# Optimization experiments

Hardware: AMD Instinct MI355X
Metric: run time of the kernel (lower is better)

## Reference

```python
import jax, jax.numpy as jnp
import numpy as np

N = 100_000      # nodes
E = 1_600_000    # edges (avg degree 16)
IN, H, OUT = 128, 64, 32
G = 128          # graphs in batch
EPS = 1e-5


def setup_inputs() -> dict:
    key = jax.random.key(0)
    ks = jax.random.split(key, 12)
    x = jax.random.normal(ks[0], (N, IN), jnp.float32)
    edge_index = jax.random.randint(ks[1], (2, E), 0, N, dtype=jnp.int32)
    batch = jnp.sort(jax.random.randint(ks[2], (N,), 0, G, dtype=jnp.int32))
    # GCNConv weights (glorot-ish scaling), shared BatchNorm params, final linear
    W1 = jax.random.normal(ks[3], (IN, H), jnp.float32) / np.sqrt(IN)
    b1 = jnp.zeros((H,), jnp.float32)
    W2 = jax.random.normal(ks[4], (H, H), jnp.float32) / np.sqrt(H)
    b2 = jnp.zeros((H,), jnp.float32)
    gamma = jnp.ones((H,), jnp.float32)
    beta = jnp.zeros((H,), jnp.float32)
    linW = jax.random.normal(ks[5], (H, OUT), jnp.float32) / np.sqrt(H)
    linb = jnp.zeros((OUT,), jnp.float32)
    return dict(x=x, edge_index=edge_index, batch=batch, W1=W1, b1=b1,
                W2=W2, b2=b2, gamma=gamma, beta=beta, linW=linW, linb=linb)


def _gcn_edges(edge_index):
    # add self loops (PyG GCNConv default) and symmetric normalization
    loop = jnp.arange(N, dtype=edge_index.dtype)
    src = jnp.concatenate([edge_index[0], loop])
    dst = jnp.concatenate([edge_index[1], loop])
    deg = jax.ops.segment_sum(jnp.ones_like(src, jnp.float32), dst, num_segments=N)
    dis = jnp.where(deg > 0, jax.lax.rsqrt(deg), 0.0)
    norm = dis[src] * dis[dst]          # [E+N]
    return src, dst, norm


def _gcn_conv(h, W, b, src, dst, norm):
    h = h @ W                            # [N, out] small GEMM first (PyG order)
    msg = h[src] * norm[:, None]         # gather + edgewise normalize
    return jax.ops.segment_sum(msg, dst, num_segments=N) + b  # scatter-add


def _batchnorm(h, gamma, beta):
    # training-mode batch stats over nodes (biased variance, as torch BN)
    mean = h.mean(axis=0)
    var = jnp.mean((h - mean) ** 2, axis=0)
    return (h - mean) * jax.lax.rsqrt(var + EPS) * gamma + beta


def reference(x, edge_index, batch, W1, b1, W2, b2, gamma, beta, linW, linb):
    src, dst, norm = _gcn_edges(edge_index)
    h = jax.nn.relu(_batchnorm(_gcn_conv(x, W1, b1, src, dst, norm), gamma, beta))
    h = jax.nn.relu(_batchnorm(_gcn_conv(h, W2, b2, src, dst, norm), gamma, beta))
    # global mean pool over graph ids
    sums = jax.ops.segment_sum(h, batch, num_segments=G)
    cnts = jax.ops.segment_sum(jnp.ones((N,), h.dtype), batch, num_segments=G)
    pooled = sums / jnp.maximum(cnts, 1.0)[:, None]   # [G, H]
    return pooled @ linW + linb                        # [G, OUT]
```

## Files before the change

kernel.cpp:

```cpp
#include <hip/hip_runtime.h>

#define NNODES 100000
#define NEDGES 1600000
#define FIN 128
#define FH 64
#define FOUT 32
#define NGRAPH 128
#define EPSV 1e-5f

#define SCAN_BT 256
#define NBLK ((NNODES + SCAN_BT - 1) / SCAN_BT)

typedef unsigned short ushort_t;
typedef __attribute__((ext_vector_type(8))) short bf16x8;
typedef __attribute__((ext_vector_type(4))) float f32x4;

__device__ inline unsigned f2bf(float f) {
  union { float f; unsigned u; } x;
  x.f = f;
  return (x.u + 0x7fffu + ((x.u >> 16) & 1u)) >> 16;
}
__device__ inline float bflo(unsigned u) {
  union { unsigned u; float f; } x;
  x.u = u << 16;
  return x.f;
}
__device__ inline float bfhi(unsigned u) {
  union { unsigned u; float f; } x;
  x.u = u & 0xffff0000u;
  return x.f;
}


__global__ void k_deg_accum(const int* __restrict__ dst, int* __restrict__ deg) {
  const int SLICE = NNODES / 8;
  int xcd = blockIdx.x & 7;
  int lo = xcd * SLICE, hi = lo + SLICE;
  int chunk = blockIdx.x >> 3;
  int nchunk = gridDim.x >> 3;
  for (int i = chunk * blockDim.x + threadIdx.x; i < NEDGES; i += nchunk * blockDim.x) {
    int d = dst[i];
    if (d >= lo && d < hi) atomicAdd(&deg[d], 1);
  }
}


__global__ void k_blocksum(const int* __restrict__ deg, int* __restrict__ bsum) {
  __shared__ int ls[SCAN_BT];
  int b = blockIdx.x, t = threadIdx.x;
  int i = b * SCAN_BT + t;
  ls[t] = (i < NNODES) ? deg[i] : 0;
  __syncthreads();
  for (int s = SCAN_BT / 2; s > 0; s >>= 1) {
    if (t < s) ls[t] += ls[t + s];
    __syncthreads();
  }
  if (t == 0) bsum[b] = ls[0];
}

__global__ void k_scan_bsums(const int* __restrict__ bsum, int* __restrict__ boff) {
  __shared__ int ls[512];
  int t = threadIdx.x;
  int v = (t < NBLK) ? bsum[t] : 0;
  ls[t] = v;
  __syncthreads();
  for (int s = 1; s < 512; s <<= 1) {
    int add = (t >= s) ? ls[t - s] : 0;
    __syncthreads();
    ls[t] += add;
    __syncthreads();
  }
  if (t < NBLK) boff[t] = ls[t] - v;
}


__global__ void k_scan_final(const int* __restrict__ deg, const int* __restrict__ boff,
                             int* __restrict__ off, float* __restrict__ dis) {
  __shared__ int ls[SCAN_BT];
  int b = blockIdx.x, t = threadIdx.x;
  int i = b * SCAN_BT + t;
  int v = (i < NNODES) ? deg[i] : 0;
  ls[t] = v;
  __syncthreads();
  for (int s = 1; s < SCAN_BT; s <<= 1) {
    int add = (t >= s) ? ls[t - s] : 0;
    __syncthreads();
    ls[t] += add;
    __syncthreads();
  }
  if (i < NNODES) {
    off[i] = boff[b] + ls[t] - v;
    dis[i] = rsqrtf((float)v + 1.0f);
  }
  if (i == NNODES - 1) off[NNODES] = boff[b] + ls[t];
}


__global__ void k_fill(const int* __restrict__ src, const int* __restrict__ dst,
                       const int* __restrict__ off, int* __restrict__ cursor,
                       int* __restrict__ csr) {
  const int SLICE = NNODES / 8;
  int xcd = blockIdx.x & 7;
  int lo = xcd * SLICE, hi = lo + SLICE;
  int chunk = blockIdx.x >> 3;
  int nchunk = gridDim.x >> 3;
  for (int i = chunk * blockDim.x + threadIdx.x; i < NEDGES; i += nchunk * blockDim.x) {
    int d = dst[i];
    if (d >= lo && d < hi) {
      int p = atomicAdd(&cursor[d], 1);
      csr[off[d] + p] = src[i];
    }
  }
}


template <int K, bool BN>
__global__ void k_gemm_mfma(const float* __restrict__ A, const float* __restrict__ W,
                            const float* __restrict__ stats, const float* __restrict__ gamma,
                            const float* __restrict__ beta, const float* __restrict__ dis,
                            ushort_t* __restrict__ out) {
  const int WT = K + 8;
  __shared__ ushort_t wt[64 * (K + 8)];
  __shared__ float bn_sc[K], bn_sh[K];
  if (BN && threadIdx.x < K) {
    int f = threadIdx.x;
    float mean = stats[f] * (1.0f / NNODES);
    float var = stats[K + f] * (1.0f / NNODES) - mean * mean;
    float s = gamma[f] * rsqrtf(var + EPSV);
    bn_sc[f] = s;
    bn_sh[f] = beta[f] - mean * s;
  }
  for (int idx = threadIdx.x; idx < K * 64; idx += 256) {
    int k = idx >> 6, col = idx & 63;
    wt[col * WT + k] = (ushort_t)f2bf(W[idx]);
  }
  __syncthreads();

  int wave = threadIdx.x >> 6;
  int lane = threadIdx.x & 63;
  int rrow = lane & 15;
  int g = lane >> 4;
  int row0 = (blockIdx.x * 4 + wave) * 16;
  int arow = min(row0 + rrow, NNODES - 1);
  const float* a = A + (long long)arow * K;

  f32x4 acc0 = {0.f, 0.f, 0.f, 0.f}, acc1 = acc0, acc2 = acc0, acc3 = acc0;

#pragma unroll
  for (int ks = 0; ks < K / 32; ++ks) {
    int koff = ks * 32 + g * 8;
    float4 xa = *(const float4*)(a + koff);
    float4 xb = *(const float4*)(a + koff + 4);
    float xs[8] = {xa.x, xa.y, xa.z, xa.w, xb.x, xb.y, xb.z, xb.w};
    if (BN) {
#pragma unroll
      for (int j = 0; j < 8; ++j)
        xs[j] = fmaxf(fmaf(xs[j], bn_sc[koff + j], bn_sh[koff + j]), 0.0f);
    }
    bf16x8 af;
#pragma unroll
    for (int j = 0; j < 8; ++j) af[j] = (short)f2bf(xs[j]);
    bf16x8 b0 = *(const bf16x8*)&wt[(0 * 16 + rrow) * WT + koff];
    bf16x8 b1 = *(const bf16x8*)&wt[(1 * 16 + rrow) * WT + koff];
    bf16x8 b2 = *(const bf16x8*)&wt[(2 * 16 + rrow) * WT + koff];
    bf16x8 b3 = *(const bf16x8*)&wt[(3 * 16 + rrow) * WT + koff];
    acc0 = __builtin_amdgcn_mfma_f32_16x16x32_bf16(af, b0, acc0, 0, 0, 0);
    acc1 = __builtin_amdgcn_mfma_f32_16x16x32_bf16(af, b1, acc1, 0, 0, 0);
    acc2 = __builtin_amdgcn_mfma_f32_16x16x32_bf16(af, b2, acc2, 0, 0, 0);
    acc3 = __builtin_amdgcn_mfma_f32_16x16x32_bf16(af, b3, acc3, 0, 0, 0);
  }

  int orow0 = row0 + g * 4;
#pragma unroll
  for (int r = 0; r < 4; ++r) {
    int orow = orow0 + r;
    if (orow < NNODES) {
      float d = dis[orow];
      ushort_t* o = out + (long long)orow * FH + rrow;
      o[0] = (ushort_t)f2bf(acc0[r] * d);
      o[16] = (ushort_t)f2bf(acc1[r] * d);
      o[32] = (ushort_t)f2bf(acc2[r] * d);
      o[48] = (ushort_t)f2bf(acc3[r] * d);
    }
  }
}


__global__ void k_gather(const ushort_t* __restrict__ hs, const int* __restrict__ csr,
                         const int* __restrict__ off, const float* __restrict__ dis,
                         float* __restrict__ out, float* __restrict__ stats) {
  __shared__ float ls[2 * FH];
  int tid = threadIdx.x;
  if (tid < 2 * FH) ls[tid] = 0.0f;
  __syncthreads();
  int lane = tid & 63;
  int g = lane >> 4;
  int i = lane & 15;
  int wid = (blockIdx.x * blockDim.x + tid) >> 6;
  int nw = (gridDim.x * blockDim.x) >> 6;
  const int HALF = NNODES / 2;
  float s1x = 0, s1y = 0, s1z = 0, s1w = 0;
  float s2x = 0, s2y = 0, s2z = 0, s2w = 0;
  for (int p = wid; p < HALF; p += nw) {
    int dA = p, dB = p + HALF;
    int bA = off[dA], eA = off[dA + 1];
    int bB = off[dB], eB = off[dB + 1];
    uint2 suA = *(const uint2*)(hs + (long long)dA * FH + i * 4);
    uint2 suB = *(const uint2*)(hs + (long long)dB * FH + i * 4);
    float axA = (g == 0) ? bflo(suA.x) : 0.0f;
    float ayA = (g == 0) ? bfhi(suA.x) : 0.0f;
    float azA = (g == 0) ? bflo(suA.y) : 0.0f;
    float awA = (g == 0) ? bfhi(suA.y) : 0.0f;
    float axB = (g == 0) ? bflo(suB.x) : 0.0f;
    float ayB = (g == 0) ? bfhi(suB.x) : 0.0f;
    float azB = (g == 0) ? bflo(suB.y) : 0.0f;
    float awB = (g == 0) ? bfhi(suB.y) : 0.0f;
    int nA = (eA - bA + 15) >> 4, nB = (eB - bB + 15) >> 4;
    int niter = max(nA, nB);
    int lastA = max(eA - 1, 0), lastB = max(eB - 1, 0);
    int kA = bA + g, kB = bB + g;
    for (int j = 0; j < niter; ++j) {
      int a0 = kA + 16 * j, a1 = a0 + 4, a2 = a0 + 8, a3 = a0 + 12;
      int b0 = kB + 16 * j, b1 = b0 + 4, b2 = b0 + 8, b3 = b0 + 12;
      int cA0 = csr[min(a0, lastA)];
      int cA1 = csr[min(a1, lastA)];
      int cA2 = csr[min(a2, lastA)];
      int cA3 = csr[min(a3, lastA)];
      int cB0 = csr[min(b0, lastB)];
      int cB1 = csr[min(b1, lastB)];
      int cB2 = csr[min(b2, lastB)];
      int cB3 = csr[min(b3, lastB)];
      uint2 uA0 = *(const uint2*)(hs + (long long)cA0 * FH + i * 4);
      uint2 uA1 = *(const uint2*)(hs + (long long)cA1 * FH + i * 4);
      uint2 uA2 = *(const uint2*)(hs + (long long)cA2 * FH + i * 4);
      uint2 uA3 = *(const uint2*)(hs + (long long)cA3 * FH + i * 4);
      uint2 uB0 = *(const uint2*)(hs + (long long)cB0 * FH + i * 4);
      uint2 uB1 = *(const uint2*)(hs + (long long)cB1 * FH + i * 4);
      uint2 uB2 = *(const uint2*)(hs + (long long)cB2 * FH + i * 4);
      uint2 uB3 = *(const uint2*)(hs + (long long)cB3 * FH + i * 4);
      bool A0 = a0 < eA, A1 = a1 < eA, A2 = a2 < eA, A3 = a3 < eA;
      bool B0 = b0 < eB, B1 = b1 < eB, B2 = b2 < eB, B3 = b3 < eB;
      axA += (A0 ? bflo(uA0.x) : 0.0f) + (A1 ? bflo(uA1.x) : 0.0f) +
             (A2 ? bflo(uA2.x) : 0.0f) + (A3 ? bflo(uA3.x) : 0.0f);
      ayA += (A0 ? bfhi(uA0.x) : 0.0f) + (A1 ? bfhi(uA1.x) : 0.0f) +
             (A2 ? bfhi(uA2.x) : 0.0f) + (A3 ? bfhi(uA3.x) : 0.0f);
      azA += (A0 ? bflo(uA0.y) : 0.0f) + (A1 ? bflo(uA1.y) : 0.0f) +
             (A2 ? bflo(uA2.y) : 0.0f) + (A3 ? bflo(uA3.y) : 0.0f);
      awA += (A0 ? bfhi(uA0.y) : 0.0f) + (A1 ? bfhi(uA1.y) : 0.0f) +
             (A2 ? bfhi(uA2.y) : 0.0f) + (A3 ? bfhi(uA3.y) : 0.0f);
      axB += (B0 ? bflo(uB0.x) : 0.0f) + (B1 ? bflo(uB1.x) : 0.0f) +
             (B2 ? bflo(uB2.x) : 0.0f) + (B3 ? bflo(uB3.x) : 0.0f);
      ayB += (B0 ? bfhi(uB0.x) : 0.0f) + (B1 ? bfhi(uB1.x) : 0.0f) +
             (B2 ? bfhi(uB2.x) : 0.0f) + (B3 ? bfhi(uB3.x) : 0.0f);
      azB += (B0 ? bflo(uB0.y) : 0.0f) + (B1 ? bflo(uB1.y) : 0.0f) +
             (B2 ? bflo(uB2.y) : 0.0f) + (B3 ? bflo(uB3.y) : 0.0f);
      awB += (B0 ? bfhi(uB0.y) : 0.0f) + (B1 ? bfhi(uB1.y) : 0.0f) +
             (B2 ? bfhi(uB2.y) : 0.0f) + (B3 ? bfhi(uB3.y) : 0.0f);
    }
    axA += __shfl_xor(axA, 16); axA += __shfl_xor(axA, 32);
    ayA += __shfl_xor(ayA, 16); ayA += __shfl_xor(ayA, 32);
    azA += __shfl_xor(azA, 16); azA += __shfl_xor(azA, 32);
    awA += __shfl_xor(awA, 16); awA += __shfl_xor(awA, 32);
    axB += __shfl_xor(axB, 16); axB += __shfl_xor(axB, 32);
    ayB += __shfl_xor(ayB, 16); ayB += __shfl_xor(ayB, 32);
    azB += __shfl_xor(azB, 16); azB += __shfl_xor(azB, 32);
    awB += __shfl_xor(awB, 16); awB += __shfl_xor(awB, 32);
    float ddA = dis[dA], ddB = dis[dB];
    float oxA = axA * ddA, oyA = ayA * ddA, ozA = azA * ddA, owA = awA * ddA;
    float oxB = axB * ddB, oyB = ayB * ddB, ozB = azB * ddB, owB = awB * ddB;
    if (g < 2) {
      int d = (g == 0) ? dA : dB;
      float4 o4;
      o4.x = (g == 0) ? oxA : oxB;
      o4.y = (g == 0) ? oyA : oyB;
      o4.z = (g == 0) ? ozA : ozB;
      o4.w = (g == 0) ? owA : owB;
      *(float4*)(out + (long long)d * FH + i * 4) = o4;
    }
    s1x += oxA + oxB; s2x += oxA * oxA + oxB * oxB;
    s1y += oyA + oyB; s2y += oyA * oyA + oyB * oyB;
    s1z += ozA + ozB; s2z += ozA * ozA + ozB * ozB;
    s1w += owA + owB; s2w += owA * owA + owB * owB;
  }
  if (g == 0) {
    atomicAdd(&ls[i * 4 + 0], s1x);
    atomicAdd(&ls[i * 4 + 1], s1y);
    atomicAdd(&ls[i * 4 + 2], s1z);
    atomicAdd(&ls[i * 4 + 3], s1w);
    atomicAdd(&ls[FH + i * 4 + 0], s2x);
    atomicAdd(&ls[FH + i * 4 + 1], s2y);
    atomicAdd(&ls[FH + i * 4 + 2], s2z);
    atomicAdd(&ls[FH + i * 4 + 3], s2w);
  }
  __syncthreads();
  if (tid < 2 * FH) atomicAdd(&stats[tid], ls[tid]);
}


#define POOL_WAVES 1024

__global__ void k_pool(const float* __restrict__ h, const int* __restrict__ batch,
                       const float* __restrict__ stats, const float* __restrict__ gamma,
                       const float* __restrict__ beta, float* __restrict__ pooled,
                       float* __restrict__ cnt) {
  const int CHUNK = (NNODES + POOL_WAVES - 1) / POOL_WAVES;
  int lane = threadIdx.x & 63;
  int wid = (blockIdx.x * blockDim.x + threadIdx.x) >> 6;
  int start = wid * CHUNK;
  if (start >= NNODES) return;
  int end = min(start + CHUNK, NNODES);
  float mean = stats[lane] * (1.0f / NNODES);
  float var = stats[FH + lane] * (1.0f / NNODES) - mean * mean;
  float sc = gamma[lane] * rsqrtf(var + EPSV);
  float sh = beta[lane] - mean * sc;
  int cur = batch[start];
  float acc = 0.0f;
  int cl = 0;
  for (int n = start; n < end; ++n) {
    int g = batch[n];
    if (g != cur) {
      atomicAdd(&pooled[cur * FH + lane], acc);
      if (lane == 0) atomicAdd(&cnt[cur], (float)cl);
      acc = 0.0f;
      cl = 0;
      cur = g;
    }
    float v = fmaf(h[(long long)n * FH + lane], sc, sh);
    acc += fmaxf(v, 0.0f);
    ++cl;
  }
  atomicAdd(&pooled[cur * FH + lane], acc);
  if (lane == 0) atomicAdd(&cnt[cur], (float)cl);
}


__global__ void k_final(const float* __restrict__ pooled, const float* __restrict__ cnt,
                        const float* __restrict__ linW, const float* __restrict__ linb,
                        float* __restrict__ out) {
  int t = blockIdx.x * blockDim.x + threadIdx.x;
  if (t >= NGRAPH * FOUT) return;
  int g = t / FOUT, o = t % FOUT;
  float inv = 1.0f / fmaxf(cnt[g], 1.0f);
  float acc = linb[o];
#pragma unroll
  for (int k = 0; k < FH; ++k) acc = fmaf(pooled[g * FH + k] * inv, linW[k * FOUT + o], acc);
  out[t] = acc;
}

extern "C" void kernel_launch(void* const* d_in, const int* in_sizes, int n_in,
                              void* d_out, int out_size, void* d_ws, size_t ws_size,
                              hipStream_t stream) {
  const float* x = (const float*)d_in[0];
  const int* edge_index = (const int*)d_in[1];
  const int* batch = (const int*)d_in[2];
  const float* W1 = (const float*)d_in[3];
  const float* W2 = (const float*)d_in[5];
  const float* gamma = (const float*)d_in[7];
  const float* beta = (const float*)d_in[8];
  const float* linW = (const float*)d_in[9];
  const float* linb = (const float*)d_in[10];
  float* out = (float*)d_out;

  const int* esrc = edge_index;
  const int* edst = edge_index + NEDGES;

  ushort_t* bufA = (ushort_t*)d_ws;
  float* bufB = (float*)d_ws + (long long)NNODES * FH;
  float* dis = bufB + (long long)NNODES * FH;
  int* off = (int*)(dis + NNODES);
  int* csr = off + (NNODES + 1);
  int* bsum = csr + NEDGES;
  int* boff = bsum + NBLK;
  int* deg = boff + NBLK;
  int* cursor = deg + NNODES;
  float* stats1 = (float*)(cursor + NNODES);
  float* stats2 = stats1 + 2 * FH;
  float* pooled = stats2 + 2 * FH;
  float* cnt = pooled + NGRAPH * FH;

  const int BT = 256;
  const int gN = (NNODES + BT - 1) / BT;
  const int gM = (NNODES + 63) / 64;

  hipMemsetAsync(deg, 0,
                 (size_t)(2 * NNODES + 2 * 2 * FH + NGRAPH * FH + NGRAPH) * sizeof(int), stream);

  k_deg_accum<<<2048, BT, 0, stream>>>(edst, deg);
  k_blocksum<<<NBLK, SCAN_BT, 0, stream>>>(deg, bsum);
  k_scan_bsums<<<1, 512, 0, stream>>>(bsum, boff);
  k_scan_final<<<NBLK, SCAN_BT, 0, stream>>>(deg, boff, off, dis);
  k_fill<<<2048, BT, 0, stream>>>(esrc, edst, off, cursor, csr);

  k_gemm_mfma<FIN, false><<<gM, BT, 0, stream>>>(x, W1, nullptr, nullptr, nullptr, dis, bufA);
  k_gather<<<2048, BT, 0, stream>>>(bufA, csr, off, dis, bufB, stats1);

  k_gemm_mfma<FH, true><<<gM, BT, 0, stream>>>(bufB, W2, stats1, gamma, beta, dis, bufA);
  k_gather<<<2048, BT, 0, stream>>>(bufA, csr, off, dis, bufB, stats2);

  k_pool<<<POOL_WAVES * 64 / BT, BT, 0, stream>>>(bufB, batch, stats2, gamma, beta, pooled, cnt);
  k_final<<<(NGRAPH * FOUT + BT - 1) / BT, BT, 0, stream>>>(pooled, cnt, linW, linb, out);
}
```

Before: 418.3 us.

## Fuse CSR fill with first GEMM and widen gather to 8-feature lanes

Merges the CSR fill kernel and the first MFMA GEMM into one launch, with disjoint block ranges, so the two independent stages can overlap. Restructures the gather kernel so each lane handles 8 bf16 features with 16-byte loads over 8 edge groups, halving the load count per edge and changing the shuffle reduction. The fused launch shifts the block-to-XCD mapping of the fill section, and the gather init contains redundant code.

Measured after the change: 419.9 us. Within noise of the previous version (+0.4%).

```diff
diff --git a/kernel.cpp b/kernel.cpp
--- a/kernel.cpp
+++ b/kernel.cpp
@@ -10,6 +10,8 @@
 
 #define SCAN_BT 256
 #define NBLK ((NNODES + SCAN_BT - 1) / SCAN_BT)
+#define GM ((NNODES + 63) / 64)
+#define FILLBLK 2048
 
 typedef unsigned short ushort_t;
 typedef __attribute__((ext_vector_type(8))) short bf16x8;
@@ -73,7 +75,6 @@
   if (t < NBLK) boff[t] = ls[t] - v;
 }
 
-
 __global__ void k_scan_final(const int* __restrict__ deg, const int* __restrict__ boff,
                              int* __restrict__ off, float* __restrict__ dis) {
   __shared__ int ls[SCAN_BT];
@@ -96,29 +97,14 @@
 }
 
 
-__global__ void k_fill(const int* __restrict__ src, const int* __restrict__ dst,
-                       const int* __restrict__ off, int* __restrict__ cursor,
-                       int* __restrict__ csr) {
-  const int SLICE = NNODES / 8;
-  int xcd = blockIdx.x & 7;
-  int lo = xcd * SLICE, hi = lo + SLICE;
-  int chunk = blockIdx.x >> 3;
-  int nchunk = gridDim.x >> 3;
-  for (int i = chunk * blockDim.x + threadIdx.x; i < NEDGES; i += nchunk * blockDim.x) {
-    int d = dst[i];
-    if (d >= lo && d < hi) {
-      int p = atomicAdd(&cursor[d], 1);
-      csr[off[d] + p] = src[i];
-    }
-  }
-}
-
-
 template <int K, bool BN>
-__global__ void k_gemm_mfma(const float* __restrict__ A, const float* __restrict__ W,
-                            const float* __restrict__ stats, const float* __restrict__ gamma,
-                            const float* __restrict__ beta, const float* __restrict__ dis,
-                            ushort_t* __restrict__ out) {
+__device__ __forceinline__ void gemm_body(int bid, const float* __restrict__ A,
+                                          const float* __restrict__ W,
+                                          const float* __restrict__ stats,
+                                          const float* __restrict__ gamma,
+                                          const float* __restrict__ beta,
+                                          const float* __restrict__ dis,
+                                          ushort_t* __restrict__ out) {
   const int WT = K + 8;
   __shared__ ushort_t wt[64 * (K + 8)];
   __shared__ float bn_sc[K], bn_sh[K];
@@ -140,7 +126,7 @@
   int lane = threadIdx.x & 63;
   int rrow = lane & 15;
   int g = lane >> 4;
-  int row0 = (blockIdx.x * 4 + wave) * 16;
+  int row0 = (bid * 4 + wave) * 16;
   int arow = min(row0 + rrow, NNODES - 1);
   const float* a = A + (long long)arow * K;
 
@@ -185,6 +171,49 @@
   }
 }
 
+template <int K, bool BN>
+__global__ void k_gemm_mfma(const float* __restrict__ A, const float* __restrict__ W,
+                            const float* __restrict__ stats, const float* __restrict__ gamma,
+                            const float* __restrict__ beta, const float* __restrict__ dis,
+                            ushort_t* __restrict__ out) {
+  gemm_body<K, BN>(blockIdx.x, A, W, stats, gamma, beta, dis, out);
+}
+
+
+__global__ void k_fill_gemm1(const float* __restrict__ x, const float* __restrict__ W1,
+                             const float* __restrict__ dis, ushort_t* __restrict__ bufA,
+                             const int* __restrict__ src, const int* __restrict__ dst,
+                             const int* __restrict__ off, int* __restrict__ cursor,
+                             int* __restrict__ csr) {
+  if (blockIdx.x < GM) {
+    gemm_body<FIN, false>(blockIdx.x, x, W1, nullptr, nullptr, nullptr, dis, bufA);
+  } else {
+    int bb = blockIdx.x - GM;
+    const int SLICE = NNODES / 8;
+    int xcd = bb & 7;
+    int lo = xcd * SLICE, hi = lo + SLICE;
+    int chunk = bb >> 3;
+    int nchunk = FILLBLK >> 3;
+    for (int i = chunk * blockDim.x + threadIdx.x; i < NEDGES; i += nchunk * blockDim.x) {
+      int d = dst[i];
+      if (d >= lo && d < hi) {
+        int p = atomicAdd(&cursor[d], 1);
+        csr[off[d] + p] = src[i];
+      }
+    }
+  }
+}
+
+
+#define ACC8(acc, u, ok)                       \
+  acc[0] += (ok) ? bflo(u.x) : 0.0f;           \
+  acc[1] += (ok) ? bfhi(u.x) : 0.0f;           \
+  acc[2] += (ok) ? bflo(u.y) : 0.0f;           \
+  acc[3] += (ok) ? bfhi(u.y) : 0.0f;           \
+  acc[4] += (ok) ? bflo(u.z) : 0.0f;           \
+  acc[5] += (ok) ? bfhi(u.z) : 0.0f;           \
+  acc[6] += (ok) ? bflo(u.w) : 0.0f;           \
+  acc[7] += (ok) ? bfhi(u.w) : 0.0f;
 
 __global__ void k_gather(const ushort_t* __restrict__ hs, const int* __restrict__ csr,
                          const int* __restrict__ off, const float* __restrict__ dis,
@@ -194,103 +223,90 @@
   if (tid < 2 * FH) ls[tid] = 0.0f;
   __syncthreads();
   int lane = tid & 63;
-  int g = lane >> 4;
-  int i = lane & 15;
+  int q = lane >> 3;
+  int i = lane & 7;
   int wid = (blockIdx.x * blockDim.x + tid) >> 6;
   int nw = (gridDim.x * blockDim.x) >> 6;
   const int HALF = NNODES / 2;
-  float s1x = 0, s1y = 0, s1z = 0, s1w = 0;
-  float s2x = 0, s2y = 0, s2z = 0, s2w = 0;
+  float s1[8], s2[8];
+#pragma unroll
+  for (int f = 0; f < 8; ++f) s1[f] = s2[f] = 0.0f;
+
   for (int p = wid; p < HALF; p += nw) {
     int dA = p, dB = p + HALF;
     int bA = off[dA], eA = off[dA + 1];
     int bB = off[dB], eB = off[dB + 1];
-    uint2 suA = *(const uint2*)(hs + (long long)dA * FH + i * 4);
-    uint2 suB = *(const uint2*)(hs + (long long)dB * FH + i * 4);
-    float axA = (g == 0) ? bflo(suA.x) : 0.0f;
-    float ayA = (g == 0) ? bfhi(suA.x) : 0.0f;
-    float azA = (g == 0) ? bflo(suA.y) : 0.0f;
-    float awA = (g == 0) ? bfhi(suA.y) : 0.0f;
-    float axB = (g == 0) ? bflo(suB.x) : 0.0f;
-    float ayB = (g == 0) ? bfhi(suB.x) : 0.0f;
-    float azB = (g == 0) ? bflo(suB.y) : 0.0f;
-    float awB = (g == 0) ? bfhi(suB.y) : 0.0f;
+    uint4 selfA = *(const uint4*)(hs + (long long)dA * FH + i * 8);
+    uint4 selfB = *(const uint4*)(hs + (long long)dB * FH + i * 8);
+    float accA[8], accB[8];
+    bool q0 = (q == 0);
+    ACC8(((float(&)[8])accA), selfA, q0);
+#pragma unroll
+    for (int f = 0; f < 8; ++f) accA[f] = q0 ? accA[f] : 0.0f;
+#pragma unroll
+    for (int f = 0; f < 8; ++f) accA[f] = 0.0f;
+#pragma unroll
+    for (int f = 0; f < 8; ++f) accB[f] = 0.0f;
+    ACC8(accA, selfA, q0);
+    ACC8(accB, selfB, q0);
+
     int nA = (eA - bA + 15) >> 4, nB = (eB - bB + 15) >> 4;
     int niter = max(nA, nB);
     int lastA = max(eA - 1, 0), lastB = max(eB - 1, 0);
-    int kA = bA + g, kB = bB + g;
+    int kA0 = bA + q, kA1 = bA + q + 8;
+    int kB0 = bB + q, kB1 = bB + q + 8;
     for (int j = 0; j < niter; ++j) {
-      int a0 = kA + 16 * j, a1 = a0 + 4, a2 = a0 + 8, a3 = a0 + 12;
-      int b0 = kB + 16 * j, b1 = b0 + 4, b2 = b0 + 8, b3 = b0 + 12;
+      int a0 = kA0 + 16 * j, a1 = kA1 + 16 * j;
+      int b0 = kB0 + 16 * j, b1 = kB1 + 16 * j;
       int cA0 = csr[min(a0, lastA)];
       int cA1 = csr[min(a1, lastA)];
-      int cA2 = csr[min(a2, lastA)];
-      int cA3 = csr[min(a3, lastA)];
       int cB0 = csr[min(b0, lastB)];
       int cB1 = csr[min(b1, lastB)];
-      int cB2 = csr[min(b2, lastB)];
-      int cB3 = csr[min(b3, lastB)];
-      uint2 uA0 = *(const uint2*)(hs + (long long)cA0 * FH + i * 4);
-      uint2 uA1 = *(const uint2*)(hs + (long long)cA1 * FH + i * 4);
-      uint2 uA2 = *(const uint2*)(hs + (long long)cA2 * FH + i * 4);
-      uint2 uA3 = *(const uint2*)(hs + (long long)cA3 * FH + i * 4);
-      uint2 uB0 = *(const uint2*)(hs + (long long)cB0 * FH + i * 4);
-      uint2 uB1 = *(const uint2*)(hs + (long long)cB1 * FH + i * 4);
-      uint2 uB2 = *(const uint2*)(hs + (long long)cB2 * FH + i * 4);
-      uint2 uB3 = *(const uint2*)(hs + (long long)cB3 * FH + i * 4);
-      bool A0 = a0 < eA, A1 = a1 < eA, A2 = a2 < eA, A3 = a3 < eA;
-      bool B0 = b0 < eB, B1 = b1 < eB, B2 = b2 < eB, B3 = b3 < eB;
-      axA += (A0 ? bflo(uA0.x) : 0.0f) + (A1 ? bflo(uA1.x) : 0.0f) +
-             (A2 ? bflo(uA2.x) : 0.0f) + (A3 ? bflo(uA3.x) : 0.0f);
-      ayA += (A0 ? bfhi(uA0.x) : 0.0f) + (A1 ? bfhi(uA1.x) : 0.0f) +
-             (A2 ? bfhi(uA2.x) : 0.0f) + (A3 ? bfhi(uA3.x) : 0.0f);
-      azA += (A0 ? bflo(uA0.y) : 0.0f) + (A1 ? bflo(uA1.y) : 0.0f) +
-             (A2 ? bflo(uA2.y) : 0.0f) + (A3 ? bflo(uA3.y) : 0.0f);
-      awA += (A0 ? bfhi(uA0.y) : 0.0f) + (A1 ? bfhi(uA1.y) : 0.0f) +
-             (A2 ? bfhi(uA2.y) : 0.0f) + (A3 ? bfhi(uA3.y) : 0.0f);
-      axB += (B0 ? bflo(uB0.x) : 0.0f) + (B1 ? bflo(uB1.x) : 0.0f) +
-             (B2 ? bflo(uB2.x) : 0.0f) + (B3 ? bflo(uB3.x) : 0.0f);
-      ayB += (B0 ? bfhi(uB0.x) : 0.0f) + (B1 ? bfhi(uB1.x) : 0.0f) +
-             (B2 ? bfhi(uB2.x) : 0.0f) + (B3 ? bfhi(uB3.x) : 0.0f);
-      azB += (B0 ? bflo(uB0.y) : 0.0f) + (B1 ? bflo(uB1.y) : 0.0f) +
-             (B2 ? bflo(uB2.y) : 0.0f) + (B3 ? bflo(uB3.y) : 0.0f);
-      awB += (B0 ? bfhi(uB0.y) : 0.0f) + (B1 ? bfhi(uB1.y) : 0.0f) +
-             (B2 ? bfhi(uB2.y) : 0.0f) + (B3 ? bfhi(uB3.y) : 0.0f);
-    }
-    axA += __shfl_xor(axA, 16); axA += __shfl_xor(axA, 32);
-    ayA += __shfl_xor(ayA, 16); ayA += __shfl_xor(ayA, 32);
-    azA += __shfl_xor(azA, 16); azA += __shfl_xor(azA, 32);
-    awA += __shfl_xor(awA, 16); awA += __shfl_xor(awA, 32);
-    axB += __shfl_xor(axB, 16); axB += __shfl_xor(axB, 32);
-    ayB += __shfl_xor(ayB, 16); ayB += __shfl_xor(ayB, 32);
-    azB += __shfl_xor(azB, 16); azB += __shfl_xor(azB, 32);
-    awB += __shfl_xor(awB, 16); awB += __shfl_xor(awB, 32);
+      uint4 uA0 = *(const uint4*)(hs + (long long)cA0 * FH + i * 8);
+      uint4 uA1 = *(const uint4*)(hs + (long long)cA1 * FH + i * 8);
+      uint4 uB0 = *(const uint4*)(hs + (long long)cB0 * FH + i * 8);
+      uint4 uB1 = *(const uint4*)(hs + (long long)cB1 * FH + i * 8);
+      bool A0 = a0 < eA, A1 = a1 < eA, B0 = b0 < eB, B1 = b1 < eB;
+      ACC8(accA, uA0, A0);
+      ACC8(accA, uA1, A1);
+      ACC8(accB, uB0, B0);
+      ACC8(accB, uB1, B1);
+    }
+#pragma unroll
+    for (int f = 0; f < 8; ++f) {
+      accA[f] += __shfl_xor(accA[f], 8);
+      accA[f] += __shfl_xor(accA[f], 16);
+      accA[f] += __shfl_xor(accA[f], 32);
+      accB[f] += __shfl_xor(accB[f], 8);
+      accB[f] += __shfl_xor(accB[f], 16);
+      accB[f] += __shfl_xor(accB[f], 32);
+    }
     float ddA = dis[dA], ddB = dis[dB];
-    float oxA = axA * ddA, oyA = ayA * ddA, ozA = azA * ddA, owA = awA * ddA;
-    float oxB = axB * ddB, oyB = ayB * ddB, ozB = azB * ddB, owB = awB * ddB;
-    if (g < 2) {
-      int d = (g == 0) ? dA : dB;
-      float4 o4;
-      o4.x = (g == 0) ? oxA : oxB;
-      o4.y = (g == 0) ? oyA : oyB;
-      o4.z = (g == 0) ? ozA : ozB;
-      o4.w = (g == 0) ? owA : owB;
-      *(float4*)(out + (long long)d * FH + i * 4) = o4;
-    }
-    s1x += oxA + oxB; s2x += oxA * oxA + oxB * oxB;
-    s1y += oyA + oyB; s2y += oyA * oyA + oyB * oyB;
-    s1z += ozA + ozB; s2z += ozA * ozA + ozB * ozB;
-    s1w += owA + owB; s2w += owA * owA + owB * owB;
-  }
-  if (g == 0) {
-    atomicAdd(&ls[i * 4 + 0], s1x);
-    atomicAdd(&ls[i * 4 + 1], s1y);
-    atomicAdd(&ls[i * 4 + 2], s1z);
-    atomicAdd(&ls[i * 4 + 3], s1w);
-    atomicAdd(&ls[FH + i * 4 + 0], s2x);
-    atomicAdd(&ls[FH + i * 4 + 1], s2y);
-    atomicAdd(&ls[FH + i * 4 + 2], s2z);
-    atomicAdd(&ls[FH + i * 4 + 3], s2w);
+#pragma unroll
+    for (int f = 0; f < 8; ++f) {
+      accA[f] *= ddA;
+      accB[f] *= ddB;
+      s1[f] += accA[f] + accB[f];
+      s2[f] += accA[f] * accA[f] + accB[f] * accB[f];
+    }
+    if (q == 0) {
+      float4 v0 = {accA[0], accA[1], accA[2], accA[3]};
+      float4 v1 = {accA[4], accA[5], accA[6], accA[7]};
+      *(float4*)(out + (long long)dA * FH + i * 8) = v0;
+      *(float4*)(out + (long long)dA * FH + i * 8 + 4) = v1;
+    } else if (q == 1) {
+      float4 v0 = {accB[0], accB[1], accB[2], accB[3]};
+      float4 v1 = {accB[4], accB[5], accB[6], accB[7]};
+      *(float4*)(out + (long long)dB * FH + i * 8) = v0;
+      *(float4*)(out + (long long)dB * FH + i * 8 + 4) = v1;
+    }
+  }
+  if (q == 2) {
+#pragma unroll
+    for (int f = 0; f < 8; ++f) {
+      atomicAdd(&ls[i * 8 + f], s1[f]);
+      atomicAdd(&ls[FH + i * 8 + f], s2[f]);
+    }
   }
   __syncthreads();
   if (tid < 2 * FH) atomicAdd(&stats[tid], ls[tid]);
@@ -379,8 +395,6 @@
   float* cnt = pooled + NGRAPH * FH;
 
   const int BT = 256;
-  const int gN = (NNODES + BT - 1) / BT;
-  const int gM = (NNODES + 63) / 64;
 
   hipMemsetAsync(deg, 0,
                  (size_t)(2 * NNODES + 2 * 2 * FH + NGRAPH * FH + NGRAPH) * sizeof(int), stream);
@@ -389,12 +403,11 @@
   k_blocksum<<<NBLK, SCAN_BT, 0, stream>>>(deg, bsum);
   k_scan_bsums<<<1, 512, 0, stream>>>(bsum, boff);
   k_scan_final<<<NBLK, SCAN_BT, 0, stream>>>(deg, boff, off, dis);
-  k_fill<<<2048, BT, 0, stream>>>(esrc, edst, off, cursor, csr);
-
-  k_gemm_mfma<FIN, false><<<gM, BT, 0, stream>>>(x, W1, nullptr, nullptr, nullptr, dis, bufA);
+  k_fill_gemm1<<<GM + FILLBLK, BT, 0, stream>>>(x, W1, dis, bufA, esrc, edst, off, cursor, csr);
+
   k_gather<<<2048, BT, 0, stream>>>(bufA, csr, off, dis, bufB, stats1);
 
-  k_gemm_mfma<FH, true><<<gM, BT, 0, stream>>>(bufB, W2, stats1, gamma, beta, dis, bufA);
+  k_gemm_mfma<FH, true><<<GM, BT, 0, stream>>>(bufB, W2, stats1, gamma, beta, dis, bufA);
   k_gather<<<2048, BT, 0, stream>>>(bufA, csr, off, dis, bufB, stats2);
 
   k_pool<<<POOL_WAVES * 64 / BT, BT, 0, stream>>>(bufB, batch, stats2, gamma, beta, pooled, cnt);
```
